# Optimization experiments

Measured on AMD Instinct MI355X. Metric: run time of the kernel, lower is better.

The kernel has to match this reference:

```python
import jax, jax.numpy as jnp
import numpy as np

N_NODES = 50000
N_EDGES = 800000
NFEAT, NHID, NCLASS = 512, 256, 64


def _glorot(key, fan_in, fan_out):
    # mimics kipf-style uniform init: U(-1/sqrt(fan_out), 1/sqrt(fan_out))
    stdv = 1.0 / np.sqrt(fan_out)
    return jax.random.uniform(key, (fan_in, fan_out), jnp.float32, -stdv, stdv)


def setup_inputs() -> dict:
    key = jax.random.key(0)
    ks = jax.random.split(key, 8)
    x = jax.random.normal(ks[0], (N_NODES, NFEAT), jnp.float32)
    edge_src = jax.random.randint(ks[1], (N_EDGES,), 0, N_NODES, jnp.int32)
    edge_dst = jax.random.randint(ks[2], (N_EDGES,), 0, N_NODES, jnp.int32)
    edge_weight = jax.random.uniform(ks[3], (N_EDGES,), jnp.float32)
    W1 = _glorot(ks[4], NFEAT, NHID)
    b1 = jax.random.uniform(ks[5], (NHID,), jnp.float32, -1.0 / np.sqrt(NHID), 1.0 / np.sqrt(NHID))
    W2 = _glorot(ks[6], NHID, NCLASS)
    b2 = jax.random.uniform(ks[7], (NCLASS,), jnp.float32, -1.0 / np.sqrt(NCLASS), 1.0 / np.sqrt(NCLASS))
    return {"x": x, "W1": W1, "b1": b1, "W2": W2, "b2": b2,
            "edge_weight": edge_weight, "edge_src": edge_src, "edge_dst": edge_dst}


def _spmm(edge_src, edge_dst, edge_weight, support):
    # adj @ support with adj given as COO edge list: out[d] += w * support[s]
    msgs = support[edge_src] * edge_weight[:, None]  # [E, F]
    return jax.ops.segment_sum(msgs, edge_dst, num_segments=N_NODES)


def reference(x, W1, b1, W2, b2, edge_weight, edge_src, edge_dst):
    # layer 1: GraphConvolution -> ReLU (dropout identity in eval mode)
    h = _spmm(edge_src, edge_dst, edge_weight, x @ W1) + b1
    h = jax.nn.relu(h)
    # layer 2: GraphConvolution -> log_softmax over classes
    logits = _spmm(edge_src, edge_dst, edge_weight, h @ W2) + b2
    return jax.nn.log_softmax(logits, axis=1)
```

## Files before the change

kernel.cpp:

```cpp
#include <hip/hip_runtime.h>
#include <cstdint>


typedef unsigned short u16;
typedef unsigned int u32;
typedef unsigned long long u64;
typedef __attribute__((ext_vector_type(8))) short bf16x8;
typedef __attribute__((ext_vector_type(4))) float f32x4;

#define N_NODES 50000
#define N_EDGES 800000
#define NFEAT 512
#define NHID 256
#define NCLASS 64
#define CSTRIDE 64

#define NBUCK 196
#define BCAP 5120
#define SCB 391
#define GB1 782
#define PW1B 512
#define PW2B 64
#define FNB 3125

__device__ __forceinline__ float bf2f(u16 h) {
    union { u32 u; float f; } c; c.u = ((u32)h) << 16; return c.f;
}
__device__ __forceinline__ u16 f2bf(float f) {
    union { float f; u32 u; } c; c.f = f;
    u32 u = c.u;
    return (u16)((u + 0x7fffu + ((u >> 16) & 1u)) >> 16);
}
__device__ __forceinline__ u32 pk2(float a, float b) {
    return (u32)f2bf(a) | ((u32)f2bf(b) << 16);
}

__device__ __forceinline__ void async16(const void* g, void* l) {
    __builtin_amdgcn_global_load_lds(
        (const __attribute__((address_space(1))) void*)(uintptr_t)g,
        (__attribute__((address_space(3))) void*)(uintptr_t)l, 16, 0, 0);
}


__global__ __launch_bounds__(256) void prep_scatter_kernel(
    const float* __restrict__ W1, u16* __restrict__ W1T,
    const float* __restrict__ W2, u16* __restrict__ W2T,
    const int* __restrict__ esrc, const int* __restrict__ edst,
    const float* __restrict__ ew, int* __restrict__ fill, u64* __restrict__ region) {
    __shared__ int cnt[NBUCK];
    __shared__ int base[NBUCK];
    int b = blockIdx.x, tid = threadIdx.x;
    if (b < SCB) {
        if (tid < NBUCK) cnt[tid] = 0;
        __syncthreads();
        int e0 = b * 2048 + tid * 8;
        int d[8], s[8], rk[8];
        float w[8];
        bool act = (e0 < N_EDGES);
        if (act) {
            int4 d0 = *(const int4*)(edst + e0),  d1 = *(const int4*)(edst + e0 + 4);
            int4 s0 = *(const int4*)(esrc + e0),  s1 = *(const int4*)(esrc + e0 + 4);
            float4 w0 = *(const float4*)(ew + e0), w1 = *(const float4*)(ew + e0 + 4);
            d[0]=d0.x; d[1]=d0.y; d[2]=d0.z; d[3]=d0.w;
            d[4]=d1.x; d[5]=d1.y; d[6]=d1.z; d[7]=d1.w;
            s[0]=s0.x; s[1]=s0.y; s[2]=s0.z; s[3]=s0.w;
            s[4]=s1.x; s[5]=s1.y; s[6]=s1.z; s[7]=s1.w;
            w[0]=w0.x; w[1]=w0.y; w[2]=w0.z; w[3]=w0.w;
            w[4]=w1.x; w[5]=w1.y; w[6]=w1.z; w[7]=w1.w;
            #pragma unroll
            for (int i = 0; i < 8; ++i)
                rk[i] = atomicAdd(&cnt[d[i] >> 8], 1);
        }
        __syncthreads();
        if (tid < NBUCK) base[tid] = atomicAdd(&fill[tid], cnt[tid]);
        __syncthreads();
        if (act) {
            #pragma unroll
            for (int i = 0; i < 8; ++i) {
                int g = d[i] >> 8;
                int pos = base[g] + rk[i];
                if (pos < BCAP) {
                    u64 en = ((u64)(d[i] & 255) << 32) |
                             (u64)((u32)s[i] | ((u32)f2bf(w[i]) << 16));
                    region[(size_t)g * BCAP + pos] = en;
                }
            }
        }
    } else if (b < SCB + PW1B) {
        int idx = (b - SCB) * 256 + tid;
        int n = idx >> 9, k = idx & 511;
        W1T[idx] = f2bf(W1[(size_t)k * NHID + n]);
    } else {
        int idx = (b - SCB - PW1B) * 256 + tid;
        int n = idx >> 8, k = idx & 255;
        W2T[idx] = f2bf(W2[(size_t)k * NCLASS + n]);
    }
}


template <int MT, int NT, int WCOLS, int K, bool ACVT>
__device__ __forceinline__ void gemm_body(const void* __restrict__ Av,
                                          const u16* __restrict__ BT,
                                          u16* __restrict__ C, int M,
                                          int bid, u16* lds) {
    constexpr int WROWS = 4 / WCOLS;
    constexpr int RT = MT / (16 * WROWS);
    constexpr int CT = NT / (16 * WCOLS);
    u16* As = lds;
    u16* Bs = lds + MT * 64;

    const int tid  = threadIdx.x;
    const int wv   = tid >> 6, lane = tid & 63;
    const int lm   = lane & 15, quad = lane >> 4;
    const int wrow = wv / WCOLS, wcol = wv % WCOLS;
    const int m0   = bid * MT;
    const int co0 = ((0 * 4 + quad) ^ (lm & 7)) * 8;
    const int co1 = ((1 * 4 + quad) ^ (lm & 7)) * 8;

    f32x4 acc[RT][CT];
    #pragma unroll
    for (int r = 0; r < RT; ++r)
        #pragma unroll
        for (int c = 0; c < CT; ++c) acc[r][c] = (f32x4){0.f, 0.f, 0.f, 0.f};

    for (int k0 = 0; k0 < K; k0 += 64) {
        if constexpr (ACVT) {
            static_assert(MT == 64, "ACVT staging assumes MT==64 (16 elems/thread)");
            const float* Af = (const float*)Av;
            int row = tid >> 2, ko = (tid & 3) * 16;
            int gr = m0 + row; if (gr > M - 1) gr = M - 1;
            const float4* gp = (const float4*)(Af + (size_t)gr * K + k0 + ko);
            float4 f0 = gp[0], f1 = gp[1], f2 = gp[2], f3 = gp[3];
            #pragma unroll
            for (int i = 0; i < NT / 32; ++i) {
                int c = i * 256 + tid;
                int n = c >> 3, kb = c & 7;
                async16(BT + (size_t)n * K + k0 + ((kb ^ (n & 7)) * 8), Bs + c * 8);
            }
            u32 p[8] = {pk2(f0.x, f0.y), pk2(f0.z, f0.w), pk2(f1.x, f1.y), pk2(f1.z, f1.w),
                        pk2(f2.x, f2.y), pk2(f2.z, f2.w), pk2(f3.x, f3.y), pk2(f3.z, f3.w)};
            int ch0 = (2 * (tid & 3))     ^ (row & 7);
            int ch1 = (2 * (tid & 3) + 1) ^ (row & 7);
            *(int4*)(As + row * 64 + ch0 * 8) = *(int4*)&p[0];
            *(int4*)(As + row * 64 + ch1 * 8) = *(int4*)&p[4];
        } else {
            const u16* A = (const u16*)Av;
            #pragma unroll
            for (int i = 0; i < NT / 32; ++i) {
                int c = i * 256 + tid;
                int n = c >> 3, kb = c & 7;
                async16(BT + (size_t)n * K + k0 + ((kb ^ (n & 7)) * 8), Bs + c * 8);
            }
            #pragma unroll
            for (int i = 0; i < MT / 32; ++i) {
                int c = i * 256 + tid;
                int row = c >> 3, kb = c & 7;
                int gr = m0 + row; if (gr > M - 1) gr = M - 1;
                async16(A + (size_t)gr * K + k0 + ((kb ^ (row & 7)) * 8), As + c * 8);
            }
        }
        __syncthreads();

        #pragma unroll
        for (int kk = 0; kk < 2; ++kk) {
            const int co = kk ? co1 : co0;
            bf16x8 af[RT], bfv[CT];
            #pragma unroll
            for (int rt = 0; rt < RT; ++rt) {
                int row = wrow * (RT * 16) + rt * 16 + lm;
                af[rt] = *(const bf16x8*)(As + row * 64 + co);
            }
            #pragma unroll
            for (int ct = 0; ct < CT; ++ct) {
                int n = wcol * CT * 16 + ct * 16 + lm;
                bfv[ct] = *(const bf16x8*)(Bs + n * 64 + co);
            }
            #pragma unroll
            for (int rt = 0; rt < RT; ++rt)
                #pragma unroll
                for (int ct = 0; ct < CT; ++ct)
                    acc[rt][ct] = __builtin_amdgcn_mfma_f32_16x16x32_bf16(
                        af[rt], bfv[ct], acc[rt][ct], 0, 0, 0);
        }
        __syncthreads();
    }

    #pragma unroll
    for (int rt = 0; rt < RT; ++rt)
        #pragma unroll
        for (int ct = 0; ct < CT; ++ct) {
            int col = wcol * CT * 16 + ct * 16 + lm;
            #pragma unroll
            for (int r = 0; r < 4; ++r) {
                int row = wrow * (RT * 16) + rt * 16 + quad * 4 + r;
                lds[row * NT + col] = f2bf(acc[rt][ct][r]);
            }
        }
    __syncthreads();
    constexpr int NC = MT * NT / 2048;
    #pragma unroll
    for (int i = 0; i < NC; ++i) {
        int c = i * 256 + tid;
        int row = (c * 8) / NT;
        if (m0 + row < M)
            *(int4*)(C + (size_t)m0 * NT + c * 8) = *(const int4*)(lds + c * 8);
    }
}


__global__ __launch_bounds__(256) void gemm1_sort_kernel(
    const float* __restrict__ x, const u16* __restrict__ W1T, u16* __restrict__ S1,
    const u64* __restrict__ region, const int* __restrict__ fill,
    u32* __restrict__ csr, int* __restrict__ deg) {
    __shared__ __align__(16) u16 lds[(64 + 256) * 64];
    int b = blockIdx.x, tid = threadIdx.x;
    if (b < NBUCK) {
        int* cnt2 = (int*)lds;
        cnt2[tid] = 0;
        __syncthreads();
        int Eb = fill[b]; if (Eb > BCAP) Eb = BCAP;
        for (int i = tid; i < Eb; i += 256) {
            u64 en = region[(size_t)b * BCAP + i];
            int dlo = (int)(en >> 32) & 255;
            int r = atomicAdd(&cnt2[dlo], 1);
            if (r < CSTRIDE)
                csr[(size_t)(b * 256 + dlo) * CSTRIDE + r] = (u32)en;
        }
        __syncthreads();
        int node = b * 256 + tid;
        if (node < N_NODES) {
            int dg = cnt2[tid]; if (dg > CSTRIDE) dg = CSTRIDE;
            deg[node] = dg;
        }
    } else {
        gemm_body<64, 256, 4, NFEAT, true>(x, W1T, S1, N_NODES, b - NBUCK, lds);
    }
}


__global__ __launch_bounds__(256) void spmm1_gemm2_kernel(
    const u16* __restrict__ S, const int* __restrict__ deg,
    const u32* __restrict__ csr, const float* __restrict__ bias1,
    const u16* __restrict__ W2T, u16* __restrict__ S2) {
    __shared__ __align__(16) u16 Hs[16 * 256];

    const int tid  = threadIdx.x;
    const int wv   = tid >> 6, lane = tid & 63;
    const int lm   = lane & 15, quad = lane >> 4;
    const int b    = blockIdx.x;

    float4 bv = *(const float4*)(bias1 + lane * 4);

    #pragma unroll
    for (int it = 0; it < 4; ++it) {
        int lrow = wv * 4 + it;
        int node = __builtin_amdgcn_readfirstlane(b * 16 + lrow);
        int beg = node * CSTRIDE;
        int end = beg + deg[node];
        float a0 = 0.f, a1 = 0.f, a2 = 0.f, a3 = 0.f;
        int j = beg;
        for (; j + 16 <= end; j += 16) {
            u32 e[16];
            #pragma unroll
            for (int i = 0; i < 16; ++i) e[i] = csr[j + i];
            ushort4 v[16];
            #pragma unroll
            for (int i = 0; i < 16; ++i)
                v[i] = *(const ushort4*)(S + (size_t)(e[i] & 0xFFFFu) * NHID + lane * 4);
            #pragma unroll
            for (int i = 0; i < 16; ++i) {
                float w = bf2f((u16)(e[i] >> 16));
                a0 += w * bf2f(v[i].x); a1 += w * bf2f(v[i].y);
                a2 += w * bf2f(v[i].z); a3 += w * bf2f(v[i].w);
            }
        }
        for (; j + 8 <= end; j += 8) {
            u32 e[8];
            #pragma unroll
            for (int i = 0; i < 8; ++i) e[i] = csr[j + i];
            ushort4 v[8];
            #pragma unroll
            for (int i = 0; i < 8; ++i)
                v[i] = *(const ushort4*)(S + (size_t)(e[i] & 0xFFFFu) * NHID + lane * 4);
            #pragma unroll
            for (int i = 0; i < 8; ++i) {
                float w = bf2f((u16)(e[i] >> 16));
                a0 += w * bf2f(v[i].x); a1 += w * bf2f(v[i].y);
                a2 += w * bf2f(v[i].z); a3 += w * bf2f(v[i].w);
            }
        }
        for (; j < end; ++j) {
            u32 e0 = csr[j];
            float w = bf2f((u16)(e0 >> 16));
            ushort4 v0 = *(const ushort4*)(S + (size_t)(e0 & 0xFFFFu) * NHID + lane * 4);
            a0 += w * bf2f(v0.x); a1 += w * bf2f(v0.y);
            a2 += w * bf2f(v0.z); a3 += w * bf2f(v0.w);
        }
        a0 = fmaxf(a0 + bv.x, 0.f);
        a1 = fmaxf(a1 + bv.y, 0.f);
        a2 = fmaxf(a2 + bv.z, 0.f);
        a3 = fmaxf(a3 + bv.w, 0.f);
        int ch = (lane >> 1) ^ (lrow & 7);
        u32* dp = (u32*)(Hs + lrow * 256 + ch * 8 + (lane & 1) * 4);
        dp[0] = pk2(a0, a1);
        dp[1] = pk2(a2, a3);
    }
    __syncthreads();

    f32x4 acc = (f32x4){0.f, 0.f, 0.f, 0.f};
    #pragma unroll
    for (int k0 = 0; k0 < NHID; k0 += 64) {
        #pragma unroll
        for (int kk = 0; kk < 2; ++kk) {
            int ca = ((k0 >> 3) + kk * 4 + quad) ^ (lm & 7);
            bf16x8 af = *(const bf16x8*)(Hs + lm * 256 + ca * 8);
            int n = wv * 16 + lm;
            bf16x8 bf = *(const bf16x8*)(W2T + (size_t)n * NHID + k0 + kk * 32 + quad * 8);
            acc = __builtin_amdgcn_mfma_f32_16x16x32_bf16(af, bf, acc, 0, 0, 0);
        }
    }
    __syncthreads();

    #pragma unroll
    for (int r = 0; r < 4; ++r) {
        int row = quad * 4 + r;
        Hs[row * 64 + wv * 16 + lm] = f2bf(acc[r]);
    }
    __syncthreads();
    *(ushort4*)(S2 + (size_t)b * 1024 + tid * 4) = *(const ushort4*)(Hs + tid * 4);
}


__global__ __launch_bounds__(256) void spmm_bias_lsm_kernel(
    const u16* __restrict__ S, const int* __restrict__ deg,
    const u32* __restrict__ csr, const float* __restrict__ bias,
    float* __restrict__ out, int n) {
    int node = blockIdx.x * 4 + (threadIdx.x >> 6);
    if (node >= n) return;
    node = __builtin_amdgcn_readfirstlane(node);
    int lane = threadIdx.x & 63;
    int beg = node * CSTRIDE;
    int end = beg + deg[node];
    float acc = 0.f;
    int j = beg;
    for (; j + 16 <= end; j += 16) {
        u32 e[16];
        #pragma unroll
        for (int i = 0; i < 16; ++i) e[i] = csr[j + i];
        u16 v[16];
        #pragma unroll
        for (int i = 0; i < 16; ++i)
            v[i] = S[(size_t)(e[i] & 0xFFFFu) * NCLASS + lane];
        #pragma unroll
        for (int i = 0; i < 16; ++i)
            acc += bf2f((u16)(e[i] >> 16)) * bf2f(v[i]);
    }
    for (; j + 8 <= end; j += 8) {
        u32 e[8];
        #pragma unroll
        for (int i = 0; i < 8; ++i) e[i] = csr[j + i];
        u16 v[8];
        #pragma unroll
        for (int i = 0; i < 8; ++i)
            v[i] = S[(size_t)(e[i] & 0xFFFFu) * NCLASS + lane];
        #pragma unroll
        for (int i = 0; i < 8; ++i)
            acc += bf2f((u16)(e[i] >> 16)) * bf2f(v[i]);
    }
    for (; j < end; ++j) {
        u32 e0 = csr[j];
        acc += bf2f((u16)(e0 >> 16)) * bf2f(S[(size_t)(e0 & 0xFFFFu) * NCLASS + lane]);
    }

    float x = acc + bias[lane];
    float m = x;
    #pragma unroll
    for (int off = 32; off > 0; off >>= 1) m = fmaxf(m, __shfl_xor(m, off));
    float e = expf(x - m);
    float ssum = e;
    #pragma unroll
    for (int off = 32; off > 0; off >>= 1) ssum += __shfl_xor(ssum, off);
    out[(size_t)node * NCLASS + lane] = x - m - logf(ssum);
}


extern "C" void kernel_launch(void* const* d_in, const int* in_sizes, int n_in,
                              void* d_out, int out_size, void* d_ws, size_t ws_size,
                              hipStream_t stream) {
    const float* x  = (const float*)d_in[0];
    const float* W1 = (const float*)d_in[1];
    const float* b1 = (const float*)d_in[2];
    const float* W2 = (const float*)d_in[3];
    const float* b2 = (const float*)d_in[4];
    const float* ew = (const float*)d_in[5];
    const int* esrc = (const int*)d_in[6];
    const int* edst = (const int*)d_in[7];
    float* out = (float*)d_out;

    char* ws = (char*)d_ws;
    size_t off = 0;
    auto take = [&](size_t bytes) -> void* {
        off = (off + 255) & ~(size_t)255;
        void* p = ws + off;
        off += bytes;
        return p;
    };
    u16* S1   = (u16*)take((size_t)N_NODES * NHID * 2);
    u16* S2   = (u16*)take((size_t)N_NODES * NCLASS * 2);
    u16* W1T  = (u16*)take((size_t)NHID * NFEAT * 2);
    u16* W2T  = (u16*)take((size_t)NCLASS * NHID * 2);
    int* deg  = (int*)take((size_t)N_NODES * 4);
    u32* csr  = (u32*)take((size_t)N_NODES * CSTRIDE * 4);
    int* fill = (int*)take((size_t)NBUCK * 4);
    u64* region = (u64*)take((size_t)NBUCK * BCAP * 8);
    (void)ws_size; (void)in_sizes; (void)n_in; (void)out_size;

    hipMemsetAsync(fill, 0, (size_t)NBUCK * 4, stream);
    prep_scatter_kernel<<<SCB + PW1B + PW2B, 256, 0, stream>>>(
        W1, W1T, W2, W2T, esrc, edst, ew, fill, region);
    gemm1_sort_kernel<<<NBUCK + GB1, 256, 0, stream>>>(
        x, W1T, S1, region, fill, csr, deg);
    spmm1_gemm2_kernel<<<FNB, 256, 0, stream>>>(S1, deg, csr, b1, W2T, S2);
    spmm_bias_lsm_kernel<<<(N_NODES + 3) / 4, 256, 0, stream>>>(
        S2, deg, csr, b2, out, N_NODES);
}
```

Baseline: 288.6 us.

## Store layer-1 support as fp8 and interleave four nodes per wave in SpMM

The GEMM1 output S1 is now quantised to a software fp8 e4m3-like byte format instead of bf16, which halves the bytes gathered per edge in the layer-1 SpMM. That SpMM decodes fp8 with bit tricks plus a 2^120 scale. Both SpMM kernels now process four nodes per wave together in chunks of eight edges, masking past each node's degree, so more gathers are in flight. The second SpMM uses 16 nodes per block. In exchange the intermediate loses precision (3-bit mantissa, clamped to ±448), and the padded chunks add wasted loads up to the maximum degree among the four nodes.

```diff
diff --git a/kernel.cpp b/kernel.cpp
--- a/kernel.cpp
+++ b/kernel.cpp
@@ -2,6 +2,7 @@
 #include <cstdint>
 
 
+typedef unsigned char u8;
 typedef unsigned short u16;
 typedef unsigned int u32;
 typedef unsigned long long u64;
@@ -33,6 +34,16 @@
 }
 __device__ __forceinline__ u32 pk2(float a, float b) {
     return (u32)f2bf(a) | ((u32)f2bf(b) << 16);
+}
+__device__ __forceinline__ float asf(u32 u) {
+    union { u32 u; float f; } c; c.u = u; return c.f;
+}
+__device__ __forceinline__ u32 f2f8(float f) {
+    f = fmaxf(fminf(f, 448.f), -448.f);
+    union { float f; u32 u; } c; c.f = f * 0x1p-120f;
+    u32 u = c.u;
+    u32 r = u + 0x7FFFFu + ((u >> 20) & 1u);
+    return ((u >> 24) & 0x80u) | ((r >> 20) & 0x7Fu);
 }
 
 __device__ __forceinline__ void async16(const void* g, void* l) {
@@ -98,118 +109,93 @@
 }
 
 
-template <int MT, int NT, int WCOLS, int K, bool ACVT>
-__device__ __forceinline__ void gemm_body(const void* __restrict__ Av,
-                                          const u16* __restrict__ BT,
-                                          u16* __restrict__ C, int M,
-                                          int bid, u16* lds) {
-    constexpr int WROWS = 4 / WCOLS;
-    constexpr int RT = MT / (16 * WROWS);
-    constexpr int CT = NT / (16 * WCOLS);
+__device__ __forceinline__ void gemm1_body(const float* __restrict__ x,
+                                           const u16* __restrict__ BT,
+                                           u8* __restrict__ C, int M,
+                                           int bid, u16* lds) {
     u16* As = lds;
-    u16* Bs = lds + MT * 64;
+    u16* Bs = lds + 64 * 64;
 
     const int tid  = threadIdx.x;
     const int wv   = tid >> 6, lane = tid & 63;
     const int lm   = lane & 15, quad = lane >> 4;
-    const int wrow = wv / WCOLS, wcol = wv % WCOLS;
-    const int m0   = bid * MT;
+    const int wcol = wv;
+    const int m0   = bid * 64;
     const int co0 = ((0 * 4 + quad) ^ (lm & 7)) * 8;
     const int co1 = ((1 * 4 + quad) ^ (lm & 7)) * 8;
 
-    f32x4 acc[RT][CT];
-    #pragma unroll
-    for (int r = 0; r < RT; ++r)
-        #pragma unroll
-        for (int c = 0; c < CT; ++c) acc[r][c] = (f32x4){0.f, 0.f, 0.f, 0.f};
-
-    for (int k0 = 0; k0 < K; k0 += 64) {
-        if constexpr (ACVT) {
-            static_assert(MT == 64, "ACVT staging assumes MT==64 (16 elems/thread)");
-            const float* Af = (const float*)Av;
-            int row = tid >> 2, ko = (tid & 3) * 16;
-            int gr = m0 + row; if (gr > M - 1) gr = M - 1;
-            const float4* gp = (const float4*)(Af + (size_t)gr * K + k0 + ko);
-            float4 f0 = gp[0], f1 = gp[1], f2 = gp[2], f3 = gp[3];
-            #pragma unroll
-            for (int i = 0; i < NT / 32; ++i) {
-                int c = i * 256 + tid;
-                int n = c >> 3, kb = c & 7;
-                async16(BT + (size_t)n * K + k0 + ((kb ^ (n & 7)) * 8), Bs + c * 8);
-            }
-            u32 p[8] = {pk2(f0.x, f0.y), pk2(f0.z, f0.w), pk2(f1.x, f1.y), pk2(f1.z, f1.w),
-                        pk2(f2.x, f2.y), pk2(f2.z, f2.w), pk2(f3.x, f3.y), pk2(f3.z, f3.w)};
-            int ch0 = (2 * (tid & 3))     ^ (row & 7);
-            int ch1 = (2 * (tid & 3) + 1) ^ (row & 7);
-            *(int4*)(As + row * 64 + ch0 * 8) = *(int4*)&p[0];
-            *(int4*)(As + row * 64 + ch1 * 8) = *(int4*)&p[4];
-        } else {
-            const u16* A = (const u16*)Av;
-            #pragma unroll
-            for (int i = 0; i < NT / 32; ++i) {
-                int c = i * 256 + tid;
-                int n = c >> 3, kb = c & 7;
-                async16(BT + (size_t)n * K + k0 + ((kb ^ (n & 7)) * 8), Bs + c * 8);
-            }
-            #pragma unroll
-            for (int i = 0; i < MT / 32; ++i) {
-                int c = i * 256 + tid;
-                int row = c >> 3, kb = c & 7;
-                int gr = m0 + row; if (gr > M - 1) gr = M - 1;
-                async16(A + (size_t)gr * K + k0 + ((kb ^ (row & 7)) * 8), As + c * 8);
-            }
-        }
+    f32x4 acc[4][4];
+    #pragma unroll
+    for (int r = 0; r < 4; ++r)
+        #pragma unroll
+        for (int c = 0; c < 4; ++c) acc[r][c] = (f32x4){0.f, 0.f, 0.f, 0.f};
+
+    for (int k0 = 0; k0 < NFEAT; k0 += 64) {
+        int row = tid >> 2, ko = (tid & 3) * 16;
+        int gr = m0 + row; if (gr > M - 1) gr = M - 1;
+        const float4* gp = (const float4*)(x + (size_t)gr * NFEAT + k0 + ko);
+        float4 f0 = gp[0], f1 = gp[1], f2 = gp[2], f3 = gp[3];
+        #pragma unroll
+        for (int i = 0; i < 8; ++i) {
+            int c = i * 256 + tid;
+            int n = c >> 3, kb = c & 7;
+            async16(BT + (size_t)n * NFEAT + k0 + ((kb ^ (n & 7)) * 8), Bs + c * 8);
+        }
+        u32 p[8] = {pk2(f0.x, f0.y), pk2(f0.z, f0.w), pk2(f1.x, f1.y), pk2(f1.z, f1.w),
+                    pk2(f2.x, f2.y), pk2(f2.z, f2.w), pk2(f3.x, f3.y), pk2(f3.z, f3.w)};
+        int ch0 = (2 * (tid & 3))     ^ (row & 7);
+        int ch1 = (2 * (tid & 3) + 1) ^ (row & 7);
+        *(int4*)(As + row * 64 + ch0 * 8) = *(int4*)&p[0];
+        *(int4*)(As + row * 64 + ch1 * 8) = *(int4*)&p[4];
         __syncthreads();
 
         #pragma unroll
         for (int kk = 0; kk < 2; ++kk) {
             const int co = kk ? co1 : co0;
-            bf16x8 af[RT], bfv[CT];
-            #pragma unroll
-            for (int rt = 0; rt < RT; ++rt) {
-                int row = wrow * (RT * 16) + rt * 16 + lm;
-                af[rt] = *(const bf16x8*)(As + row * 64 + co);
-            }
-            #pragma unroll
-            for (int ct = 0; ct < CT; ++ct) {
-                int n = wcol * CT * 16 + ct * 16 + lm;
+            bf16x8 af[4], bfv[4];
+            #pragma unroll
+            for (int rt = 0; rt < 4; ++rt)
+                af[rt] = *(const bf16x8*)(As + (rt * 16 + lm) * 64 + co);
+            #pragma unroll
+            for (int ct = 0; ct < 4; ++ct) {
+                int n = wcol * 64 + ct * 16 + lm;
                 bfv[ct] = *(const bf16x8*)(Bs + n * 64 + co);
             }
             #pragma unroll
-            for (int rt = 0; rt < RT; ++rt)
+            for (int rt = 0; rt < 4; ++rt)
                 #pragma unroll
-                for (int ct = 0; ct < CT; ++ct)
+                for (int ct = 0; ct < 4; ++ct)
                     acc[rt][ct] = __builtin_amdgcn_mfma_f32_16x16x32_bf16(
                         af[rt], bfv[ct], acc[rt][ct], 0, 0, 0);
         }
         __syncthreads();
     }
 
-    #pragma unroll
-    for (int rt = 0; rt < RT; ++rt)
-        #pragma unroll
-        for (int ct = 0; ct < CT; ++ct) {
-            int col = wcol * CT * 16 + ct * 16 + lm;
+    u8* lds8 = (u8*)lds;
+    #pragma unroll
+    for (int rt = 0; rt < 4; ++rt)
+        #pragma unroll
+        for (int ct = 0; ct < 4; ++ct) {
+            int col = wcol * 64 + ct * 16 + lm;
             #pragma unroll
             for (int r = 0; r < 4; ++r) {
-                int row = wrow * (RT * 16) + rt * 16 + quad * 4 + r;
-                lds[row * NT + col] = f2bf(acc[rt][ct][r]);
+                int row = rt * 16 + quad * 4 + r;
+                lds8[row * 256 + col] = (u8)f2f8(acc[rt][ct][r]);
             }
         }
     __syncthreads();
-    constexpr int NC = MT * NT / 2048;
-    #pragma unroll
-    for (int i = 0; i < NC; ++i) {
+    #pragma unroll
+    for (int i = 0; i < 4; ++i) {
         int c = i * 256 + tid;
-        int row = (c * 8) / NT;
+        int row = c >> 4, ch = c & 15;
         if (m0 + row < M)
-            *(int4*)(C + (size_t)m0 * NT + c * 8) = *(const int4*)(lds + c * 8);
+            *(int4*)(C + (size_t)(m0 + row) * 256 + ch * 16) = *(const int4*)(lds8 + c * 16);
     }
 }
 
 
 __global__ __launch_bounds__(256) void gemm1_sort_kernel(
-    const float* __restrict__ x, const u16* __restrict__ W1T, u16* __restrict__ S1,
+    const float* __restrict__ x, const u16* __restrict__ W1T, u8* __restrict__ S8,
     const u64* __restrict__ region, const int* __restrict__ fill,
     u32* __restrict__ csr, int* __restrict__ deg) {
     __shared__ __align__(16) u16 lds[(64 + 256) * 64];
@@ -233,13 +219,13 @@
             deg[node] = dg;
         }
     } else {
-        gemm_body<64, 256, 4, NFEAT, true>(x, W1T, S1, N_NODES, b - NBUCK, lds);
+        gemm1_body(x, W1T, S8, N_NODES, b - NBUCK, lds);
     }
 }
 
 
 __global__ __launch_bounds__(256) void spmm1_gemm2_kernel(
-    const u16* __restrict__ S, const int* __restrict__ deg,
+    const u8* __restrict__ S8, const int* __restrict__ deg,
     const u32* __restrict__ csr, const float* __restrict__ bias1,
     const u16* __restrict__ W2T, u16* __restrict__ S2) {
     __shared__ __align__(16) u16 Hs[16 * 256];
@@ -251,55 +237,57 @@
 
     float4 bv = *(const float4*)(bias1 + lane * 4);
 
-    #pragma unroll
-    for (int it = 0; it < 4; ++it) {
-        int lrow = wv * 4 + it;
-        int node = __builtin_amdgcn_readfirstlane(b * 16 + lrow);
-        int beg = node * CSTRIDE;
-        int end = beg + deg[node];
-        float a0 = 0.f, a1 = 0.f, a2 = 0.f, a3 = 0.f;
-        int j = beg;
-        for (; j + 16 <= end; j += 16) {
-            u32 e[16];
-            #pragma unroll
-            for (int i = 0; i < 16; ++i) e[i] = csr[j + i];
-            ushort4 v[16];
-            #pragma unroll
-            for (int i = 0; i < 16; ++i)
-                v[i] = *(const ushort4*)(S + (size_t)(e[i] & 0xFFFFu) * NHID + lane * 4);
-            #pragma unroll
-            for (int i = 0; i < 16; ++i) {
-                float w = bf2f((u16)(e[i] >> 16));
-                a0 += w * bf2f(v[i].x); a1 += w * bf2f(v[i].y);
-                a2 += w * bf2f(v[i].z); a3 += w * bf2f(v[i].w);
-            }
-        }
-        for (; j + 8 <= end; j += 8) {
-            u32 e[8];
-            #pragma unroll
-            for (int i = 0; i < 8; ++i) e[i] = csr[j + i];
-            ushort4 v[8];
+    int begs[4], degs[4];
+    int maxd = 0;
+    #pragma unroll
+    for (int n = 0; n < 4; ++n) {
+        int node = __builtin_amdgcn_readfirstlane(b * 16 + wv * 4 + n);
+        begs[n] = node * CSTRIDE;
+        degs[n] = deg[node];
+        maxd = max(maxd, degs[n]);
+    }
+
+    float a[4][4];
+    #pragma unroll
+    for (int n = 0; n < 4; ++n)
+        #pragma unroll
+        for (int k = 0; k < 4; ++k) a[n][k] = 0.f;
+
+    for (int kb = 0; kb < maxd; kb += 8) {
+        u32 e[4][8];
+        #pragma unroll
+        for (int n = 0; n < 4; ++n)
+            #pragma unroll
+            for (int i = 0; i < 8; ++i) {
+                u32 t = csr[begs[n] + kb + i];
+                e[n][i] = (kb + i < degs[n]) ? t : 0u;
+            }
+        u32 q[4][8];
+        #pragma unroll
+        for (int n = 0; n < 4; ++n)
             #pragma unroll
             for (int i = 0; i < 8; ++i)
-                v[i] = *(const ushort4*)(S + (size_t)(e[i] & 0xFFFFu) * NHID + lane * 4);
+                q[n][i] = *(const u32*)(S8 + (size_t)(e[n][i] & 0xFFFFu) * NHID + lane * 4);
+        #pragma unroll
+        for (int n = 0; n < 4; ++n)
             #pragma unroll
             for (int i = 0; i < 8; ++i) {
-                float w = bf2f((u16)(e[i] >> 16));
-                a0 += w * bf2f(v[i].x); a1 += w * bf2f(v[i].y);
-                a2 += w * bf2f(v[i].z); a3 += w * bf2f(v[i].w);
-            }
-        }
-        for (; j < end; ++j) {
-            u32 e0 = csr[j];
-            float w = bf2f((u16)(e0 >> 16));
-            ushort4 v0 = *(const ushort4*)(S + (size_t)(e0 & 0xFFFFu) * NHID + lane * 4);
-            a0 += w * bf2f(v0.x); a1 += w * bf2f(v0.y);
-            a2 += w * bf2f(v0.z); a3 += w * bf2f(v0.w);
-        }
-        a0 = fmaxf(a0 + bv.x, 0.f);
-        a1 = fmaxf(a1 + bv.y, 0.f);
-        a2 = fmaxf(a2 + bv.z, 0.f);
-        a3 = fmaxf(a3 + bv.w, 0.f);
+                float w = bf2f((u16)(e[n][i] >> 16)) * 0x1p120f;
+                u32 qq = q[n][i];
+                a[n][0] += w * asf(((qq & 0x80u) << 24) | ((qq & 0x7Fu) << 20));
+                a[n][1] += w * asf(((qq & 0x8000u) << 16) | ((qq & 0x7F00u) << 12));
+                a[n][2] += w * asf(((qq & 0x800000u) << 8) | ((qq & 0x7F0000u) << 4));
+                a[n][3] += w * asf((qq & 0x80000000u) | ((qq & 0x7F000000u) >> 4));
+            }
+    }
+
+    #pragma unroll
+    for (int n = 0; n < 4; ++n) {
+        int lrow = wv * 4 + n;
+        float a0 = fmaxf(a[n][0] + bv.x, 0.f);
+        float a1 = fmaxf(a[n][1] + bv.y, 0.f);
+        float a2 = fmaxf(a[n][2] + bv.z, 0.f);
+        float a3 = fmaxf(a[n][3] + bv.w, 0.f);
         int ch = (lane >> 1) ^ (lrow & 7);
         u32* dp = (u32*)(Hs + lrow * 256 + ch * 8 + (lane & 1) * 4);
         dp[0] = pk2(a0, a1);
@@ -334,53 +322,58 @@
 __global__ __launch_bounds__(256) void spmm_bias_lsm_kernel(
     const u16* __restrict__ S, const int* __restrict__ deg,
     const u32* __restrict__ csr, const float* __restrict__ bias,
-    float* __restrict__ out, int n) {
-    int node = blockIdx.x * 4 + (threadIdx.x >> 6);
-    if (node >= n) return;
-    node = __builtin_amdgcn_readfirstlane(node);
-    int lane = threadIdx.x & 63;
-    int beg = node * CSTRIDE;
-    int end = beg + deg[node];
-    float acc = 0.f;
-    int j = beg;
-    for (; j + 16 <= end; j += 16) {
-        u32 e[16];
-        #pragma unroll
-        for (int i = 0; i < 16; ++i) e[i] = csr[j + i];
-        u16 v[16];
-        #pragma unroll
-        for (int i = 0; i < 16; ++i)
-            v[i] = S[(size_t)(e[i] & 0xFFFFu) * NCLASS + lane];
-        #pragma unroll
-        for (int i = 0; i < 16; ++i)
-            acc += bf2f((u16)(e[i] >> 16)) * bf2f(v[i]);
-    }
-    for (; j + 8 <= end; j += 8) {
-        u32 e[8];
-        #pragma unroll
-        for (int i = 0; i < 8; ++i) e[i] = csr[j + i];
-        u16 v[8];
-        #pragma unroll
-        for (int i = 0; i < 8; ++i)
-            v[i] = S[(size_t)(e[i] & 0xFFFFu) * NCLASS + lane];
-        #pragma unroll
-        for (int i = 0; i < 8; ++i)
-            acc += bf2f((u16)(e[i] >> 16)) * bf2f(v[i]);
-    }
-    for (; j < end; ++j) {
-        u32 e0 = csr[j];
-        acc += bf2f((u16)(e0 >> 16)) * bf2f(S[(size_t)(e0 & 0xFFFFu) * NCLASS + lane]);
-    }
-
-    float x = acc + bias[lane];
-    float m = x;
-    #pragma unroll
-    for (int off = 32; off > 0; off >>= 1) m = fmaxf(m, __shfl_xor(m, off));
-    float e = expf(x - m);
-    float ssum = e;
-    #pragma unroll
-    for (int off = 32; off > 0; off >>= 1) ssum += __shfl_xor(ssum, off);
-    out[(size_t)node * NCLASS + lane] = x - m - logf(ssum);
+    float* __restrict__ out) {
+    const int tid = threadIdx.x;
+    const int wv = tid >> 6, lane = tid & 63;
+    const int b = blockIdx.x;
+
+    int begs[4], degs[4];
+    int maxd = 0;
+    #pragma unroll
+    for (int n = 0; n < 4; ++n) {
+        int node = __builtin_amdgcn_readfirstlane(b * 16 + wv * 4 + n);
+        begs[n] = node * CSTRIDE;
+        degs[n] = deg[node];
+        maxd = max(maxd, degs[n]);
+    }
+
+    float acc[4] = {0.f, 0.f, 0.f, 0.f};
+    for (int kb = 0; kb < maxd; kb += 8) {
+        u32 e[4][8];
+        #pragma unroll
+        for (int n = 0; n < 4; ++n)
+            #pragma unroll
+            for (int i = 0; i < 8; ++i) {
+                u32 t = csr[begs[n] + kb + i];
+                e[n][i] = (kb + i < degs[n]) ? t : 0u;
+            }
+        u16 v[4][8];
+        #pragma unroll
+        for (int n = 0; n < 4; ++n)
+            #pragma unroll
+            for (int i = 0; i < 8; ++i)
+                v[n][i] = S[(size_t)(e[n][i] & 0xFFFFu) * NCLASS + lane];
+        #pragma unroll
+        for (int n = 0; n < 4; ++n)
+            #pragma unroll
+            for (int i = 0; i < 8; ++i)
+                acc[n] += bf2f((u16)(e[n][i] >> 16)) * bf2f(v[n][i]);
+    }
+
+    float bl = bias[lane];
+    #pragma unroll
+    for (int n = 0; n < 4; ++n) {
+        int node = b * 16 + wv * 4 + n;
+        float x = acc[n] + bl;
+        float m = x;
+        #pragma unroll
+        for (int off = 32; off > 0; off >>= 1) m = fmaxf(m, __shfl_xor(m, off));
+        float e = expf(x - m);
+        float ssum = e;
+        #pragma unroll
+        for (int off = 32; off > 0; off >>= 1) ssum += __shfl_xor(ssum, off);
+        out[(size_t)node * NCLASS + lane] = x - m - logf(ssum);
+    }
 }
 
 
@@ -405,7 +398,7 @@
         off += bytes;
         return p;
     };
-    u16* S1   = (u16*)take((size_t)N_NODES * NHID * 2);
+    u8*  S8   = (u8*)take((size_t)N_NODES * NHID);
     u16* S2   = (u16*)take((size_t)N_NODES * NCLASS * 2);
     u16* W1T  = (u16*)take((size_t)NHID * NFEAT * 2);
     u16* W2T  = (u16*)take((size_t)NCLASS * NHID * 2);
@@ -419,8 +412,7 @@
     prep_scatter_kernel<<<SCB + PW1B + PW2B, 256, 0, stream>>>(
         W1, W1T, W2, W2T, esrc, edst, ew, fill, region);
     gemm1_sort_kernel<<<NBUCK + GB1, 256, 0, stream>>>(
-        x, W1T, S1, region, fill, csr, deg);
-    spmm1_gemm2_kernel<<<FNB, 256, 0, stream>>>(S1, deg, csr, b1, W2T, S2);
-    spmm_bias_lsm_kernel<<<(N_NODES + 3) / 4, 256, 0, stream>>>(
-        S2, deg, csr, b2, out, N_NODES);
-}
+        x, W1T, S8, region, fill, csr, deg);
+    spmm1_gemm2_kernel<<<FNB, 256, 0, stream>>>(S8, deg, csr, b1, W2T, S2);
+    spmm_bias_lsm_kernel<<<FNB, 256, 0, stream>>>(S2, deg, csr, b2, out);
+}
```

Result: no change. 291.0 us (+0.8%).
